# Kernel optimization log

Measured on AMD Instinct MI355X. Metric: run time of the kernel, lower is better.

Reference implementation:

```python
import jax, jax.numpy as jnp
import numpy as np

NUM_HEADS = 12
WS = 7
LN_EPS = 1e-5


def _layernorm(x, g, b):
    mu = jnp.mean(x, axis=-1, keepdims=True)
    var = jnp.var(x, axis=-1, keepdims=True)
    return (x - mu) * jax.lax.rsqrt(var + LN_EPS) * g + b


def setup_inputs() -> dict:
    key = jax.random.key(0)
    ks = jax.random.split(key, 6)
    B, win_num, n, C = 32, 64, 50, 384
    x = jax.random.normal(ks[0], (B, win_num, n, C), dtype=jnp.float32)
    std = 0.02
    w_qkv = jax.random.normal(ks[1], (3 * C, C), dtype=jnp.float32) * std  # DSA_qkv (no bias)
    w_qk = jax.random.normal(ks[2], (2 * C, C), dtype=jnp.float32) * std   # PSA_qk (no bias)
    ln_g = jnp.ones((C,), dtype=jnp.float32)
    ln_b = jnp.zeros((C,), dtype=jnp.float32)
    w_proj = jax.random.normal(ks[3], (C, C), dtype=jnp.float32) * std
    b_proj = jnp.zeros((C,), dtype=jnp.float32)
    return {"x": x, "H": 56, "W": 56, "w_qkv": w_qkv, "w_qk": w_qk,
            "ln_g": ln_g, "ln_b": ln_b, "w_proj": w_proj, "b_proj": b_proj}


def reference(x, H, W, w_qkv, w_qk, ln_g, ln_b, w_proj, b_proj):
    B, win_num, n, C = x.shape
    h = NUM_HEADS
    d = C // h
    scale = d ** -0.5
    ws = WS
    hg, wg = -(-H // ws), -(-W // ws)

    # ---- DSA: local window attention over (win_size+1) tokens ----
    qkv = (x @ w_qkv.T).reshape(B, win_num, n, 3, h, d)
    q, k, v = jnp.moveaxis(qkv, 3, 0)
    attn = jnp.einsum('bwqhd,bwkhd->bwhqk', q, k) * scale
    attn = jax.nn.softmax(attn, axis=-1)
    out = jnp.einsum('bwhqk,bwkhd->bwqhd', attn, v).reshape(B, win_num, n, C)
    out = out + x

    # split window summary tokens from window contents
    win_tok = out[:, :, 0, :]
    ax = out[:, :, 1:, :]
    win_tok = jax.nn.gelu(_layernorm(win_tok, ln_g, ln_b), approximate=False)

    # ---- PSA: global attention over window tokens ----
    pqk = (win_tok @ w_qk.T).reshape(B, win_num, 2, h, d)
    pq, pk = jnp.moveaxis(pqk, 2, 0)
    pattn = jnp.einsum('bwhd,bvhd->bhwv', pq, pk) * scale
    pattn = jax.nn.softmax(pattn, axis=-1)
    ax_r = ax.reshape(B, win_num, ws * ws, h, d)
    psa = jnp.einsum('bhwv,bvshd->bwshd', pattn, ax_r).reshape(B, win_num, ws * ws, C)
    out = psa + ax

    # ---- window reverse ----
    out = out.reshape(B, hg, wg, ws, ws, C).swapaxes(2, 3).reshape(B, hg * ws, wg * ws, C)
    out = out[:, :H, :W, :].reshape(B, H * W, C)
    return out @ w_proj.T + b_proj
```

## Files before the change

kernel.cpp:

```cpp
#include <hip/hip_runtime.h>
#include <cstdint>
#include <cstddef>

#define B_   32
#define WN   64
#define NT   50
#define C_   384
#define NH   12
#define HD   32
#define SCALE 0.17677669529663687f

typedef float  f32x4  __attribute__((ext_vector_type(4)));
typedef __bf16 bf16x8 __attribute__((ext_vector_type(8)));

__device__ __forceinline__ float bf2f(unsigned short u) {
  union { unsigned int u; float f; } v; v.u = ((unsigned int)u) << 16; return v.f;
}
__device__ __forceinline__ unsigned short f2bf(float f) {
  union { float f; unsigned int u; } v; v.f = f;
  unsigned int r = v.u + 0x7FFFu + ((v.u >> 16) & 1u);
  return (unsigned short)(r >> 16);
}

__device__ __forceinline__ void gload_lds16(const void* g, void* l) {
  __builtin_amdgcn_global_load_lds(
      (const __attribute__((address_space(1))) void*)g,
      (__attribute__((address_space(3))) void*)l, 16, 0, 0);
}

__global__ __launch_bounds__(256) void cvt_bf16_k(const float* __restrict__ src,
                                                  unsigned short* __restrict__ dst,
                                                  int nquad) {
  int i = blockIdx.x * 256 + threadIdx.x;
  if (i < nquad) {
    float4 v = ((const float4*)src)[i];
    ushort4 o;
    o.x = f2bf(v.x); o.y = f2bf(v.y); o.z = f2bf(v.z); o.w = f2bf(v.w);
    ((ushort4*)dst)[i] = o;
  }
}

template<bool OUT_BF16, bool HAS_BIAS>
__global__ __launch_bounds__(256) void gemm128_k(
    const unsigned short* __restrict__ A,
    const unsigned short* __restrict__ W,
    const float* __restrict__ bias,
    void* __restrict__ Out, int M, int N, int K)
{
  __shared__ unsigned short As[128 * 32];
  __shared__ unsigned short Bs[128 * 32];
  const int n0 = blockIdx.x * 128;
  const int m0 = blockIdx.y * 128;
  const int t  = threadIdx.x;
  const int lane = t & 63, wv = t >> 6;
  const int ln = lane & 15, kq = (lane >> 4) << 3;
  const int wm = (wv >> 1) << 6, wn = (wv & 1) << 6;

  const int row1 = t >> 2;
  const int ce1  = (t & 3) << 3;
  const size_t arow_a = (size_t)(m0 + row1) * K + ce1;
  const size_t arow_b = (size_t)(n0 + row1) * K + ce1;
  unsigned short* lA0 = As + row1 * 32 + ce1;
  unsigned short* lB0 = Bs + row1 * 32 + ce1;

  f32x4 acc[4][4];
#pragma unroll
  for (int i = 0; i < 4; ++i)
#pragma unroll
    for (int j = 0; j < 4; ++j) acc[i][j] = (f32x4){0.f, 0.f, 0.f, 0.f};

  const int nkb = K >> 5;
  for (int kb = 0; kb < nkb; ++kb) {
    const int k0 = kb << 5;
    if (kb) __syncthreads();
    gload_lds16(A + arow_a + k0,                 lA0);
    gload_lds16(A + arow_a + (size_t)64 * K + k0, lA0 + 64 * 32);
    gload_lds16(W + arow_b + k0,                 lB0);
    gload_lds16(W + arow_b + (size_t)64 * K + k0, lB0 + 64 * 32);
    __syncthreads();

    bf16x8 af[4], bf[4];
#pragma unroll
    for (int i = 0; i < 4; ++i) af[i] = *(const bf16x8*)&As[(wm + i * 16 + ln) * 32 + kq];
#pragma unroll
    for (int j = 0; j < 4; ++j) bf[j] = *(const bf16x8*)&Bs[(wn + j * 16 + ln) * 32 + kq];
#pragma unroll
    for (int i = 0; i < 4; ++i)
#pragma unroll
      for (int j = 0; j < 4; ++j)
        acc[i][j] = __builtin_amdgcn_mfma_f32_16x16x32_bf16(af[i], bf[j], acc[i][j], 0, 0, 0);
  }

  const int orow = (lane >> 4) << 2;
#pragma unroll
  for (int i = 0; i < 4; ++i)
#pragma unroll
    for (int j = 0; j < 4; ++j) {
      int gn = n0 + wn + j * 16 + ln;
      float bb = HAS_BIAS ? bias[gn] : 0.f;
#pragma unroll
      for (int r = 0; r < 4; ++r) {
        int gm = m0 + wm + i * 16 + orow + r;
        float v = acc[i][j][r] + bb;
        if (OUT_BF16) ((unsigned short*)Out)[(size_t)gm * N + gn] = f2bf(v);
        else          ((float*)Out)[(size_t)gm * N + gn] = v;
      }
    }
}

template<bool OUT_BF16, bool HAS_BIAS>
__global__ __launch_bounds__(256) void gemm_bf16_k(
    const unsigned short* __restrict__ A,
    const unsigned short* __restrict__ W,
    const float* __restrict__ bias,
    void* __restrict__ Out, int M, int N, int K)
{
  __shared__ unsigned short As[64][40];
  __shared__ unsigned short Bs[64][40];
  const int n0 = blockIdx.x * 64;
  const int m0 = blockIdx.y * 64;
  const int t  = threadIdx.x;
  const int srow = t >> 2;
  const int sseg = (t & 3) << 3;
  const int lane = t & 63;
  const int wv = t >> 6;
  const int wm = (wv >> 1) << 5;
  const int wn = (wv & 1) << 5;
  const int lr = lane & 15;
  const int kq = (lane >> 4) << 3;

  f32x4 acc[2][2] = {{{0.f,0.f,0.f,0.f},{0.f,0.f,0.f,0.f}},
                     {{0.f,0.f,0.f,0.f},{0.f,0.f,0.f,0.f}}};

  const int nkb = K >> 5;
  for (int kb = 0; kb < nkb; ++kb) {
    const int k0 = kb << 5;
    *(uint4*)&As[srow][sseg] = *(const uint4*)(A + (size_t)(m0 + srow) * K + k0 + sseg);
    *(uint4*)&Bs[srow][sseg] = *(const uint4*)(W + (size_t)(n0 + srow) * K + k0 + sseg);
    __syncthreads();
    bf16x8 a0 = *(const bf16x8*)&As[wm + lr][kq];
    bf16x8 a1 = *(const bf16x8*)&As[wm + 16 + lr][kq];
    bf16x8 b0 = *(const bf16x8*)&Bs[wn + lr][kq];
    bf16x8 b1 = *(const bf16x8*)&Bs[wn + 16 + lr][kq];
    acc[0][0] = __builtin_amdgcn_mfma_f32_16x16x32_bf16(a0, b0, acc[0][0], 0, 0, 0);
    acc[0][1] = __builtin_amdgcn_mfma_f32_16x16x32_bf16(a0, b1, acc[0][1], 0, 0, 0);
    acc[1][0] = __builtin_amdgcn_mfma_f32_16x16x32_bf16(a1, b0, acc[1][0], 0, 0, 0);
    acc[1][1] = __builtin_amdgcn_mfma_f32_16x16x32_bf16(a1, b1, acc[1][1], 0, 0, 0);
    __syncthreads();
  }
  const int orow = (lane >> 4) << 2;
#pragma unroll
  for (int i = 0; i < 2; ++i)
#pragma unroll
    for (int j = 0; j < 2; ++j)
#pragma unroll
      for (int r = 0; r < 4; ++r) {
        int gm = m0 + wm + i * 16 + orow + r;
        int gn = n0 + wn + j * 16 + lr;
        float v = acc[i][j][r];
        if (HAS_BIAS) v += bias[gn];
        if (OUT_BF16) ((unsigned short*)Out)[(size_t)gm * N + gn] = f2bf(v);
        else          ((float*)Out)[(size_t)gm * N + gn] = v;
      }
}

__global__ __launch_bounds__(256) void attn_win_k(
    const unsigned short* __restrict__ qkv,
    const unsigned short* __restrict__ xb,
    unsigned short* __restrict__ outA)
{
  const int w = blockIdx.x, b = blockIdx.y;
  const int t = threadIdx.x;
  const int lane = t & 63, wv = t >> 6;
  const int ln = lane & 15, hi = lane >> 4;

  __shared__ unsigned short Qs[64][40];
  __shared__ unsigned short Ks[64][40];
  __shared__ unsigned short Vt[32][72];
  __shared__ unsigned short Ps[64][72];

  const size_t win = (size_t)(b * WN + w);
  const size_t qkvbase = win * NT * 1152;
  const size_t obase = win * NT * C_;

  for (int h = 0; h < NH; ++h) {
    __syncthreads();
    {
      const int n = t >> 2, seg = (t & 3) << 3;
      uint4 qv = {0,0,0,0}, kv = {0,0,0,0}, vv = {0,0,0,0};
      if (n < NT) {
        const unsigned short* p = qkv + qkvbase + (size_t)n * 1152 + h * HD + seg;
        qv = *(const uint4*)p;
        kv = *(const uint4*)(p + C_);
        vv = *(const uint4*)(p + 2 * C_);
      }
      *(uint4*)&Qs[n][seg] = qv;
      *(uint4*)&Ks[n][seg] = kv;
      const unsigned short* vs = (const unsigned short*)&vv;
#pragma unroll
      for (int j = 0; j < 8; ++j) Vt[seg + j][n] = vs[j];
    }
    __syncthreads();

    f32x4 s[4];
    {
      bf16x8 aq = *(const bf16x8*)&Qs[wv * 16 + ln][hi * 8];
#pragma unroll
      for (int nt = 0; nt < 4; ++nt) {
        bf16x8 bk = *(const bf16x8*)&Ks[nt * 16 + ln][hi * 8];
        s[nt] = __builtin_amdgcn_mfma_f32_16x16x32_bf16(aq, bk, (f32x4){0.f,0.f,0.f,0.f}, 0, 0, 0);
      }
    }

#pragma unroll
    for (int r = 0; r < 4; ++r) {
      float m = -1e30f;
#pragma unroll
      for (int nt = 0; nt < 4; ++nt) {
        float val = s[nt][r] * SCALE;
        s[nt][r] = val;
        if (nt * 16 + ln < NT) m = fmaxf(m, val);
      }
#pragma unroll
      for (int o = 1; o < 16; o <<= 1) m = fmaxf(m, __shfl_xor(m, o));
      float e[4]; float sum = 0.f;
#pragma unroll
      for (int nt = 0; nt < 4; ++nt) {
        e[nt] = (nt * 16 + ln < NT) ? __expf(s[nt][r] - m) : 0.f;
        sum += e[nt];
      }
#pragma unroll
      for (int o = 1; o < 16; o <<= 1) sum += __shfl_xor(sum, o);
      float inv = 1.f / sum;
      int q = wv * 16 + hi * 4 + r;
#pragma unroll
      for (int nt = 0; nt < 4; ++nt)
        Ps[q][nt * 16 + ln] = f2bf(e[nt] * inv);
    }

    f32x4 o0 = {0.f,0.f,0.f,0.f}, o1 = {0.f,0.f,0.f,0.f};
#pragma unroll
    for (int kb = 0; kb < 2; ++kb) {
      bf16x8 bp  = *(const bf16x8*)&Ps[wv * 16 + ln][kb * 32 + hi * 8];
      bf16x8 av0 = *(const bf16x8*)&Vt[ln][kb * 32 + hi * 8];
      bf16x8 av1 = *(const bf16x8*)&Vt[16 + ln][kb * 32 + hi * 8];
      o0 = __builtin_amdgcn_mfma_f32_16x16x32_bf16(av0, bp, o0, 0, 0, 0);
      o1 = __builtin_amdgcn_mfma_f32_16x16x32_bf16(av1, bp, o1, 0, 0, 0);
    }

    const int q = wv * 16 + ln;
    if (q < NT) {
      const unsigned short* xr = xb + obase + (size_t)q * C_ + h * HD;
      unsigned short* orow = outA + obase + (size_t)q * C_ + h * HD;
      ushort4 x0 = *(const ushort4*)(xr + hi * 4);
      ushort4 x1 = *(const ushort4*)(xr + 16 + hi * 4);
      ushort4 r0, r1;
      r0.x = f2bf(o0[0] + bf2f(x0.x)); r0.y = f2bf(o0[1] + bf2f(x0.y));
      r0.z = f2bf(o0[2] + bf2f(x0.z)); r0.w = f2bf(o0[3] + bf2f(x0.w));
      r1.x = f2bf(o1[0] + bf2f(x1.x)); r1.y = f2bf(o1[1] + bf2f(x1.y));
      r1.z = f2bf(o1[2] + bf2f(x1.z)); r1.w = f2bf(o1[3] + bf2f(x1.w));
      *(ushort4*)(orow + hi * 4) = r0;
      *(ushort4*)(orow + 16 + hi * 4) = r1;
    }
  }
}

__global__ __launch_bounds__(64) void ln_gelu_k(
    const unsigned short* __restrict__ outA,
    const float* __restrict__ g, const float* __restrict__ beta,
    unsigned short* __restrict__ wt)
{
  const int row = blockIdx.x;
  const int t = threadIdx.x;
  const size_t base = (size_t)row * NT * C_;
  float v[6];
  float s = 0.f, s2 = 0.f;
#pragma unroll
  for (int i = 0; i < 6; ++i) {
    float xv = bf2f(outA[base + t + i * 64]);
    v[i] = xv; s += xv; s2 += xv * xv;
  }
#pragma unroll
  for (int off = 1; off < 64; off <<= 1) {
    s  += __shfl_xor(s, off);
    s2 += __shfl_xor(s2, off);
  }
  const float mu = s * (1.f / 384.f);
  const float var = s2 * (1.f / 384.f) - mu * mu;
  const float rinv = rsqrtf(var + 1e-5f);
#pragma unroll
  for (int i = 0; i < 6; ++i) {
    int c = t + i * 64;
    float y = (v[i] - mu) * rinv * g[c] + beta[c];
    float ge = 0.5f * y * (1.f + erff(y * 0.70710678118654752f));
    wt[(size_t)row * C_ + c] = f2bf(ge);
  }
}

__global__ __launch_bounds__(64) void pool_attn_k(
    const float* __restrict__ pqk, float* __restrict__ pattn)
{
  const int h = blockIdx.x;
  const int b = blockIdx.y;
  const int t = threadIdx.x;
  __shared__ float qs[64][32];
  __shared__ float ks[64][32];
  __shared__ float L[64][64];
  for (int idx = t; idx < 64 * 32; idx += 64) {
    int n = idx >> 5, dd = idx & 31;
    int sw = dd ^ (((n >> 3) & 7) << 2);
    size_t base = ((size_t)(b * WN + n)) * (2 * C_) + h * HD + dd;
    qs[n][sw] = pqk[base];
    ks[n][sw] = pqk[base + C_];
  }
  __syncthreads();
  const int ti = t >> 3, tj = t & 7;
  const int i0 = ti << 3, j0 = tj << 3;
  const int swi = ti << 2, swj = tj << 2;
  {
    float acc[8][8];
#pragma unroll
    for (int r = 0; r < 8; ++r)
#pragma unroll
      for (int c = 0; c < 8; ++c) acc[r][c] = 0.f;
#pragma unroll
    for (int d0 = 0; d0 < 32; d0 += 4) {
      float4 qv[8], kv[8];
#pragma unroll
      for (int r = 0; r < 8; ++r) qv[r] = *(const float4*)&qs[i0 + r][d0 ^ swi];
#pragma unroll
      for (int c = 0; c < 8; ++c) kv[c] = *(const float4*)&ks[j0 + c][d0 ^ swj];
#pragma unroll
      for (int r = 0; r < 8; ++r)
#pragma unroll
        for (int c = 0; c < 8; ++c)
          acc[r][c] += qv[r].x * kv[c].x + qv[r].y * kv[c].y + qv[r].z * kv[c].z + qv[r].w * kv[c].w;
    }
#pragma unroll
    for (int r = 0; r < 8; ++r)
#pragma unroll
      for (int c4 = 0; c4 < 2; ++c4) {
        float4 o;
        o.x = acc[r][c4 * 4 + 0] * SCALE; o.y = acc[r][c4 * 4 + 1] * SCALE;
        o.z = acc[r][c4 * 4 + 2] * SCALE; o.w = acc[r][c4 * 4 + 3] * SCALE;
        *(float4*)&L[i0 + r][(j0 + c4 * 4) ^ swi] = o;
      }
  }
  __syncthreads();
  {
    const int sw = (t >> 3) << 2;
    float m = -1e30f;
    for (int j = 0; j < 64; ++j) m = fmaxf(m, L[t][j ^ sw]);
    float sum = 0.f;
    for (int j = 0; j < 64; ++j) { float e = __expf(L[t][j ^ sw] - m); L[t][j ^ sw] = e; sum += e; }
    float inv = 1.f / sum;
    float* dst = pattn + (((size_t)b * NH + h) * 64 + t) * 64;
    for (int j = 0; j < 64; ++j) dst[j] = L[t][j ^ sw] * inv;
  }
}

__global__ __launch_bounds__(256) void pool_sa_k(
    const float* __restrict__ pattn,
    const unsigned short* __restrict__ outA,
    unsigned short* __restrict__ Y)
{
  const int tile = blockIdx.x;
  const int h = blockIdx.y;
  const int b = blockIdx.z;
  const int t = threadIdx.x;
  __shared__ float P[64][65];
  __shared__ float AXT[64][132];
  int limit = 1568 - tile * 128; if (limit > 128) limit = 128;

  {
    const float* src = pattn + ((size_t)b * NH + h) * 4096;
    for (int idx = t; idx < 4096; idx += 256) P[idx >> 6][idx & 63] = src[idx];
  }
  for (int idx = t; idx < 8192; idx += 256) {
    int v = idx >> 7, cc = idx & 127;
    float val = 0.f;
    if (cc < limit) {
      int ch = tile * 128 + cc;
      int s = ch >> 5, dd = ch & 31;
      val = bf2f(outA[((size_t)(b * WN + v) * NT + 1 + s) * C_ + h * HD + dd]);
    }
    AXT[v][cc] = val;
  }
  __syncthreads();

  const int ccq = t & 7;
  const int wi = t >> 3;
  const int w0 = wi, w1 = wi + 32;
  float a0[4][4], a1[4][4];
#pragma unroll
  for (int ch = 0; ch < 4; ++ch)
#pragma unroll
    for (int e = 0; e < 4; ++e) { a0[ch][e] = 0.f; a1[ch][e] = 0.f; }

  for (int v = 0; v < 64; ++v) {
    float p0 = P[w0][v], p1 = P[w1][v];
#pragma unroll
    for (int ch = 0; ch < 4; ++ch) {
      float4 ax = *(const float4*)&AXT[v][ch * 32 + ccq * 4];
      a0[ch][0] += p0 * ax.x; a0[ch][1] += p0 * ax.y; a0[ch][2] += p0 * ax.z; a0[ch][3] += p0 * ax.w;
      a1[ch][0] += p1 * ax.x; a1[ch][1] += p1 * ax.y; a1[ch][2] += p1 * ax.z; a1[ch][3] += p1 * ax.w;
    }
  }
#pragma unroll
  for (int ch = 0; ch < 4; ++ch) {
    int ccb = ch * 32 + ccq * 4;
    if (ccb < limit) {
      int chd = tile * 128 + ccb;
      int s = chd >> 5, dd = chd & 31;
      int srow2 = s / 7, scol = s - srow2 * 7;
      int col = h * HD + dd;
      ushort4 r0, r1;
      r0.x = f2bf(a0[ch][0] + AXT[w0][ccb + 0]);
      r0.y = f2bf(a0[ch][1] + AXT[w0][ccb + 1]);
      r0.z = f2bf(a0[ch][2] + AXT[w0][ccb + 2]);
      r0.w = f2bf(a0[ch][3] + AXT[w0][ccb + 3]);
      r1.x = f2bf(a1[ch][0] + AXT[w1][ccb + 0]);
      r1.y = f2bf(a1[ch][1] + AXT[w1][ccb + 1]);
      r1.z = f2bf(a1[ch][2] + AXT[w1][ccb + 2]);
      r1.w = f2bf(a1[ch][3] + AXT[w1][ccb + 3]);
      int hgi = w0 >> 3, wgi = w0 & 7;
      size_t yi = ((size_t)b * 3136 + (hgi * 7 + srow2) * 56 + wgi * 7 + scol) * C_ + col;
      *(ushort4*)&Y[yi] = r0;
      hgi = w1 >> 3; wgi = w1 & 7;
      yi = ((size_t)b * 3136 + (hgi * 7 + srow2) * 56 + wgi * 7 + scol) * C_ + col;
      *(ushort4*)&Y[yi] = r1;
    }
  }
}

extern "C" void kernel_launch(void* const* d_in, const int* in_sizes, int n_in,
                              void* d_out, int out_size, void* d_ws, size_t ws_size,
                              hipStream_t stream)
{
  (void)in_sizes; (void)n_in; (void)out_size; (void)ws_size;
  const float* x      = (const float*)d_in[0];
  const float* w_qkv  = (const float*)d_in[3];
  const float* w_qk   = (const float*)d_in[4];
  const float* ln_g   = (const float*)d_in[5];
  const float* ln_b   = (const float*)d_in[6];
  const float* w_proj = (const float*)d_in[7];
  const float* b_proj = (const float*)d_in[8];
  float* out = (float*)d_out;

  char* ws = (char*)d_ws;
  size_t off = 0;
  auto alloc = [&](size_t bytes) { size_t o = off; off += (bytes + 255) & ~(size_t)255; return o; };
  const size_t M1 = (size_t)B_ * WN * NT;
  const size_t M7 = (size_t)B_ * 3136;
  unsigned short* qkv    = (unsigned short*)(ws + alloc(M1 * 1152 * 2));
  unsigned short* xb     = (unsigned short*)(ws + alloc(M1 * C_ * 2));
  unsigned short* outA   = (unsigned short*)(ws + alloc(M1 * C_ * 2));
  unsigned short* wqkvb  = (unsigned short*)(ws + alloc(1152 * 384 * 2));
  unsigned short* wqkb   = (unsigned short*)(ws + alloc(768 * 384 * 2));
  unsigned short* wprojb = (unsigned short*)(ws + alloc(384 * 384 * 2));
  unsigned short* wt     = (unsigned short*)(ws + alloc(2048 * 384 * 2));
  float* pqk             = (float*)(ws + alloc(2048 * 768 * 4));
  float* pattn           = (float*)(ws + alloc((size_t)B_ * NH * 64 * 64 * 4));
  unsigned short* Y = xb;

  int q;
  q = (int)(M1 * C_ / 4);
  cvt_bf16_k<<<(q + 255) / 256, 256, 0, stream>>>(x, xb, q);
  q = 1152 * 384 / 4;
  cvt_bf16_k<<<(q + 255) / 256, 256, 0, stream>>>(w_qkv, wqkvb, q);
  q = 768 * 384 / 4;
  cvt_bf16_k<<<(q + 255) / 256, 256, 0, stream>>>(w_qk, wqkb, q);
  q = 384 * 384 / 4;
  cvt_bf16_k<<<(q + 255) / 256, 256, 0, stream>>>(w_proj, wprojb, q);

  gemm128_k<true, false><<<dim3(1152 / 128, M1 / 128), 256, 0, stream>>>(
      xb, wqkvb, nullptr, qkv, (int)M1, 1152, 384);
  attn_win_k<<<dim3(WN, B_), 256, 0, stream>>>(qkv, xb, outA);
  ln_gelu_k<<<2048, 64, 0, stream>>>(outA, ln_g, ln_b, wt);
  gemm_bf16_k<false, false><<<dim3(768 / 64, 2048 / 64), 256, 0, stream>>>(
      wt, wqkb, nullptr, pqk, 2048, 768, 384);
  pool_attn_k<<<dim3(NH, B_), 64, 0, stream>>>(pqk, pattn);
  pool_sa_k<<<dim3(13, NH, B_), 256, 0, stream>>>(pattn, outA, Y);
  gemm128_k<false, true><<<dim3(384 / 128, M7 / 128), 256, 0, stream>>>(
      Y, wprojb, b_proj, out, (int)M7, 384, 384);
}
```

Before: 796.8 us.

## Rewrite pooled window attention apply with bf16 MFMA and split-precision probabilities

Replaces the scalar FP32 FMA loop in the pooled-attention apply kernel with 16x16x32 bf16 MFMA instructions. The attention probabilities are split into high and low bf16 parts so precision stays close to FP32. Window tokens are staged transposed and swizzled in LDS, and each block now covers one row of the 7x7 window (7 tiles instead of 13). This targets ALU-bound scalar work in pool_sa, at the cost of a more complex LDS layout and scattered 2-byte output stores.

```diff
diff --git a/kernel.cpp b/kernel.cpp
--- a/kernel.cpp
+++ b/kernel.cpp
@@ -359,77 +359,102 @@
   }
 }
 
-__global__ __launch_bounds__(256) void pool_sa_k(
+__global__ __launch_bounds__(256) void pool_sa_mfma_k(
     const float* __restrict__ pattn,
     const unsigned short* __restrict__ outA,
     unsigned short* __restrict__ Y)
 {
-  const int tile = blockIdx.x;
-  const int h = blockIdx.y;
-  const int b = blockIdx.z;
-  const int t = threadIdx.x;
-  __shared__ float P[64][65];
-  __shared__ float AXT[64][132];
-  int limit = 1568 - tile * 128; if (limit > 128) limit = 128;
+  const int tt = blockIdx.x;
+  const int h  = blockIdx.y;
+  const int b  = blockIdx.z;
+  const int t  = threadIdx.x;
+
+  __shared__ unsigned short Ph[64][72];
+  __shared__ unsigned short Pl[64][72];
+  __shared__ unsigned short AXT[224][72];
 
   {
-    const float* src = pattn + ((size_t)b * NH + h) * 4096;
-    for (int idx = t; idx < 4096; idx += 256) P[idx >> 6][idx & 63] = src[idx];
-  }
-  for (int idx = t; idx < 8192; idx += 256) {
-    int v = idx >> 7, cc = idx & 127;
-    float val = 0.f;
-    if (cc < limit) {
-      int ch = tile * 128 + cc;
-      int s = ch >> 5, dd = ch & 31;
-      val = bf2f(outA[((size_t)(b * WN + v) * NT + 1 + s) * C_ + h * HD + dd]);
-    }
-    AXT[v][cc] = val;
+    const float4* src = (const float4*)(pattn + ((size_t)b * NH + h) * 4096);
+#pragma unroll
+    for (int i = 0; i < 4; ++i) {
+      int idx = t + i * 256;
+      int row = idx >> 4, seg = (idx & 15) << 2;
+      float4 p = src[idx];
+      float pv[4] = {p.x, p.y, p.z, p.w};
+      unsigned short hs[4], ls[4];
+#pragma unroll
+      for (int e = 0; e < 4; ++e) {
+        hs[e] = f2bf(pv[e]);
+        ls[e] = f2bf(pv[e] - bf2f(hs[e]));
+      }
+      ushort4 hv, lv;
+      hv.x = hs[0]; hv.y = hs[1]; hv.z = hs[2]; hv.w = hs[3];
+      lv.x = ls[0]; lv.y = ls[1]; lv.z = ls[2]; lv.w = ls[3];
+      *(ushort4*)&Ph[row][seg] = hv;
+      *(ushort4*)&Pl[row][seg] = lv;
+    }
+  }
+
+  {
+    const unsigned short* axb = outA + ((size_t)(b * WN) * NT + 1 + tt * 7) * C_ + h * HD;
+    for (int idx = t; idx < 896; idx += 256) {
+      int v2 = idx / 28;
+      int c  = idx - v2 * 28;
+      int v  = v2 << 1;
+      int s  = c >> 2, d8 = (c & 3) << 3;
+      const unsigned short* p0 = axb + (size_t)v * (NT * C_) + s * C_ + d8;
+      uint4 a0 = *(const uint4*)p0;
+      uint4 a1 = *(const uint4*)(p0 + NT * C_);
+      int cp = ((v2 >> 2) + (c & 7)) & 7;
+      int bo = cp * 8 + (v2 & 3) * 2;
+      unsigned int aw[4] = {a0.x, a0.y, a0.z, a0.w};
+      unsigned int bw[4] = {a1.x, a1.y, a1.z, a1.w};
+      int r0 = c << 3;
+#pragma unroll
+      for (int jj = 0; jj < 4; ++jj) {
+        unsigned int w0 = (aw[jj] & 0xffffu) | (bw[jj] << 16);
+        unsigned int w1 = (aw[jj] >> 16) | (bw[jj] & 0xffff0000u);
+        *(unsigned int*)&AXT[r0 + jj * 2    ][bo] = w0;
+        *(unsigned int*)&AXT[r0 + jj * 2 + 1][bo] = w1;
+      }
+    }
   }
   __syncthreads();
 
-  const int ccq = t & 7;
-  const int wi = t >> 3;
-  const int w0 = wi, w1 = wi + 32;
-  float a0[4][4], a1[4][4];
-#pragma unroll
-  for (int ch = 0; ch < 4; ++ch)
-#pragma unroll
-    for (int e = 0; e < 4; ++e) { a0[ch][e] = 0.f; a1[ch][e] = 0.f; }
-
-  for (int v = 0; v < 64; ++v) {
-    float p0 = P[w0][v], p1 = P[w1][v];
-#pragma unroll
-    for (int ch = 0; ch < 4; ++ch) {
-      float4 ax = *(const float4*)&AXT[v][ch * 32 + ccq * 4];
-      a0[ch][0] += p0 * ax.x; a0[ch][1] += p0 * ax.y; a0[ch][2] += p0 * ax.z; a0[ch][3] += p0 * ax.w;
-      a1[ch][0] += p1 * ax.x; a1[ch][1] += p1 * ax.y; a1[ch][2] += p1 * ax.z; a1[ch][3] += p1 * ax.w;
-    }
-  }
-#pragma unroll
-  for (int ch = 0; ch < 4; ++ch) {
-    int ccb = ch * 32 + ccq * 4;
-    if (ccb < limit) {
-      int chd = tile * 128 + ccb;
-      int s = chd >> 5, dd = chd & 31;
-      int srow2 = s / 7, scol = s - srow2 * 7;
-      int col = h * HD + dd;
-      ushort4 r0, r1;
-      r0.x = f2bf(a0[ch][0] + AXT[w0][ccb + 0]);
-      r0.y = f2bf(a0[ch][1] + AXT[w0][ccb + 1]);
-      r0.z = f2bf(a0[ch][2] + AXT[w0][ccb + 2]);
-      r0.w = f2bf(a0[ch][3] + AXT[w0][ccb + 3]);
-      r1.x = f2bf(a1[ch][0] + AXT[w1][ccb + 0]);
-      r1.y = f2bf(a1[ch][1] + AXT[w1][ccb + 1]);
-      r1.z = f2bf(a1[ch][2] + AXT[w1][ccb + 2]);
-      r1.w = f2bf(a1[ch][3] + AXT[w1][ccb + 3]);
-      int hgi = w0 >> 3, wgi = w0 & 7;
-      size_t yi = ((size_t)b * 3136 + (hgi * 7 + srow2) * 56 + wgi * 7 + scol) * C_ + col;
-      *(ushort4*)&Y[yi] = r0;
-      hgi = w1 >> 3; wgi = w1 & 7;
-      yi = ((size_t)b * 3136 + (hgi * 7 + srow2) * 56 + wgi * 7 + scol) * C_ + col;
-      *(ushort4*)&Y[yi] = r1;
-    }
+  const int lane = t & 63, wv = t >> 6;
+  const int ln = lane & 15, hi = lane >> 4;
+
+  bf16x8 afh[2], afl[2];
+#pragma unroll
+  for (int kb = 0; kb < 2; ++kb) {
+    afh[kb] = *(const bf16x8*)&Ph[wv * 16 + ln][kb * 32 + hi * 8];
+    afl[kb] = *(const bf16x8*)&Pl[wv * 16 + ln][kb * 32 + hi * 8];
+  }
+
+  const int wbase  = wv * 16 + hi * 4;
+  const int whi    = wbase >> 3;
+  const int wlo    = wbase & 7;
+  const int wchunk = wbase >> 3;
+  unsigned short* yb = Y + ((size_t)b * 3136 + ((size_t)whi * 7 + tt) * 56) * C_ + h * HD;
+
+#pragma unroll
+  for (int j = 0; j < 14; ++j) {
+    const int row = j * 16 + ln;
+    const int g = (row >> 3) & 7;
+    f32x4 acc = {0.f, 0.f, 0.f, 0.f};
+#pragma unroll
+    for (int kb = 0; kb < 2; ++kb) {
+      bf16x8 bfr = *(const bf16x8*)&AXT[row][((kb * 4 + hi + g) & 7) * 8];
+      acc = __builtin_amdgcn_mfma_f32_16x16x32_bf16(afh[kb], bfr, acc, 0, 0, 0);
+      acc = __builtin_amdgcn_mfma_f32_16x16x32_bf16(afl[kb], bfr, acc, 0, 0, 0);
+    }
+    ushort4 rx = *(const ushort4*)&AXT[row][((wchunk + g) & 7) * 8 + (wbase & 7)];
+    const unsigned short rr[4] = {rx.x, rx.y, rx.z, rx.w};
+    const int sl = row >> 5, d = row & 31;
+    unsigned short* yp = yb + (size_t)(wlo * 7 + sl) * C_ + d;
+#pragma unroll
+    for (int r = 0; r < 4; ++r)
+      yp[(size_t)r * 7 * C_] = f2bf(acc[r] + bf2f(rr[r]));
   }
 }
 
@@ -480,7 +505,7 @@
   gemm_bf16_k<false, false><<<dim3(768 / 64, 2048 / 64), 256, 0, stream>>>(
       wt, wqkb, nullptr, pqk, 2048, 768, 384);
   pool_attn_k<<<dim3(NH, B_), 64, 0, stream>>>(pqk, pattn);
-  pool_sa_k<<<dim3(13, NH, B_), 256, 0, stream>>>(pattn, outA, Y);
+  pool_sa_mfma_k<<<dim3(7, NH, B_), 256, 0, stream>>>(pattn, outA, Y);
   gemm128_k<false, true><<<dim3(384 / 128, M7 / 128), 256, 0, stream>>>(
       Y, wprojb, b_proj, out, (int)M7, 384, 384);
 }
```

Result: faster. 689.6 us (-13.5%).
